# Kernel optimization log

Hardware: AMD Instinct MI355X
Metric: run time of the kernel (lower is better)

Reference implementation:

```python
import jax, jax.numpy as jnp
import numpy as np


def setup_inputs() -> dict:
    key = jax.random.key(0)
    ks = jax.random.split(key, 9)
    B, D_in, H, C = 32768, 784, 256, 10
    def lin(k, fan_in, shape):
        return jax.random.normal(k, shape, dtype=jnp.float32) / np.sqrt(fan_in).astype(np.float32)
    return {
        "x": jax.random.normal(ks[0], (B, D_in), dtype=jnp.float32),
        "W1": lin(ks[1], D_in, (H, D_in)),
        "b1": lin(ks[2], D_in, (H,)),
        "W2": lin(ks[3], H, (H, H)),
        "b2": lin(ks[4], H, (H,)),
        "W3": lin(ks[5], H, (H, H)),
        "b3": lin(ks[6], H, (H,)),
        "W4": lin(ks[7], H, (C, H)),
        "b4": lin(ks[8], H, (C,)),
    }


def reference(x, W1, b1, W2, b2, W3, b3, W4, b4):
    # MLPHeb.forward_with_coactivations:
    #   prev_act = (input > 0); at each activation point (after each ReLU and
    #   at the final Linear), curr_act = (x > 0) and coactivation buffer
    #   accumulates sum_s outer(prev_act[s], curr_act[s]) == prev_act.T @ curr_act.
    act = lambda t: (t > 0).astype(t.dtype)

    a0 = act(x)                              # [B, 784]
    h1 = jax.nn.relu(x @ W1.T + b1)          # [B, 256]
    a1 = act(h1)
    c0 = a0.T @ a1                           # [784, 256]

    h2 = jax.nn.relu(h1 @ W2.T + b2)
    a2 = act(h2)
    c1 = a1.T @ a2                           # [256, 256]

    h3 = jax.nn.relu(h2 @ W3.T + b3)
    a3 = act(h3)
    c2 = a2.T @ a3                           # [256, 256]

    logits = h3 @ W4.T + b4                  # [B, 10] (last layer counts as activation point)
    a4 = act(logits)
    c3 = a3.T @ a4                           # [256, 10]

    return logits, c0, c1, c2, c3
```

## Files before the change

kernel.cpp:

```cpp
#include <hip/hip_runtime.h>
#include <hip/hip_bf16.h>

typedef unsigned short u16;
typedef unsigned long long u64;
typedef __bf16 bf16x8 __attribute__((ext_vector_type(8)));
typedef float f32x4 __attribute__((ext_vector_type(4)));

__device__ __forceinline__ void async16(const void* g, void* l) {
  __builtin_amdgcn_global_load_lds((const __attribute__((address_space(1))) void*)g,
                                   (__attribute__((address_space(3))) void*)l, 16, 0, 0);
}
__device__ __forceinline__ u16 f2bf(float f) {
  __hip_bfloat16 h = __float2bfloat16(f);
  u16 u; __builtin_memcpy(&u, &h, 2); return u;
}

__global__ __launch_bounds__(256) void convert_all(
    const float* __restrict__ W1, const float* __restrict__ W2,
    const float* __restrict__ W3, const float* __restrict__ W4,
    u16* __restrict__ w1b, u16* __restrict__ w2b,
    u16* __restrict__ w3b, u16* __restrict__ w4b) {
  int bx = blockIdx.x;
  const float* src; u16* dst; int R, C, Cp, base;
  if (bx < 800)       { src = W1; dst = w1b; R = 256; C = 784; Cp = 800; base = 0; }
  else if (bx < 1056) { src = W2; dst = w2b; R = 256; C = 256; Cp = 256; base = 800; }
  else if (bx < 1312) { src = W3; dst = w3b; R = 256; C = 256; Cp = 256; base = 1056; }
  else                { src = W4; dst = w4b; R = 10;  C = 256; Cp = 256; base = 1312; }
  int idx = (bx - base) * 256 + threadIdx.x;
  int r = idx / Cp, c = idx - r * Cp;
  float v = (r < R && c < C) ? src[(size_t)r * C + c] : 0.0f;
  dst[idx] = f2bf(v);
}

__global__ __launch_bounds__(512, 4) void fwd_fused(
    const float* __restrict__ x,
    const u16* __restrict__ W1b, const float* __restrict__ b1,
    const u16* __restrict__ W2b, const float* __restrict__ b2,
    const u16* __restrict__ W3b, const float* __restrict__ b3,
    const u16* __restrict__ W4b, const float* __restrict__ b4,
    float* __restrict__ out,
    u64* __restrict__ bits0, u64* __restrict__ bits1,
    u64* __restrict__ bits2, u64* __restrict__ bits3,
    u64* __restrict__ bits4) {

  __shared__ __align__(16) u16 hbuf[8 * 64 * 40];
  __shared__ __align__(16) u16 Wt[2][256 * 32];
  __shared__ __align__(16) float Ls[64 * 12];

  const int tid = threadIdx.x;
  const int lane = tid & 63, wv = tid >> 6;
  const int lm = lane & 15, q = lane >> 4;
  const int m0 = blockIdx.x * 64;
  const int wm = (wv & 1) * 32;
  const int wn = (wv >> 1) * 64;

  auto stageW = [&](const u16* W, int K, int kc, u16* dst) {
    #pragma unroll
    for (int i = 0; i < 2; i++) {
      int seg = i * 512 + tid;
      int n = seg >> 2, kq = seg & 3;
      async16(W + (size_t)n * K + kc * 32 + kq * 8, dst + seg * 8);
    }
  };
  auto stageW4 = [&]() {
    if (tid < 512) async16(W4b + tid * 8, Wt[1] + tid * 8);
  };
  auto epilogue = [&](f32x4 (&acc)[2][4], const float* __restrict__ bias) {
    #pragma unroll
    for (int mi = 0; mi < 2; mi++) {
      int row = wm + mi * 16 + lm;
      #pragma unroll
      for (int ni = 0; ni < 4; ni++) {
        int col = wn + ni * 16 + q * 4;
        float4 bv = *(const float4*)(bias + col);
        float h0 = acc[mi][ni][0] + bv.x; h0 = h0 > 0.0f ? h0 : 0.0f;
        float h1 = acc[mi][ni][1] + bv.y; h1 = h1 > 0.0f ? h1 : 0.0f;
        float h2 = acc[mi][ni][2] + bv.z; h2 = h2 > 0.0f ? h2 : 0.0f;
        float h3 = acc[mi][ni][3] + bv.w; h3 = h3 > 0.0f ? h3 : 0.0f;
        ushort4 o = {f2bf(h0), f2bf(h1), f2bf(h2), f2bf(h3)};
        int kt = col >> 5, cin = col & 31;
        *(ushort4*)(hbuf + kt * 2560 + row * 40 + cin) = o;
      }
    }
  };
  auto ballot_pass = [&](u64* bits) {
    u64 my = 0;
    #pragma unroll
    for (int g = 0; g < 4; g++) {
      ushort4 v0 = *(const ushort4*)(hbuf + wv * 2560 + lane * 40 + g * 8);
      ushort4 v1 = *(const ushort4*)(hbuf + wv * 2560 + lane * 40 + g * 8 + 4);
      u16 s[8] = {v0.x, v0.y, v0.z, v0.w, v1.x, v1.y, v1.z, v1.w};
      #pragma unroll
      for (int j = 0; j < 8; j++) {
        u64 m = __ballot(s[j] != 0);
        if (lane == g * 8 + j) my = m;
      }
    }
    if (lane < 32) bits[(size_t)blockIdx.x * 256 + wv * 32 + lane] = my;
  };

  {
    f32x4 acc[2][4] = {};
    float4 xv[2][2];
    bf16x8 hA[2];
    const int arow = m0 + wm + lm;

    auto loadX = [&](int kc) {
      int col = kc * 32 + q * 8;
      bool ok = col + 7 < 784;
      #pragma unroll
      for (int mi = 0; mi < 2; mi++) {
        if (ok) {
          const float* src = x + (size_t)(arow + mi * 16) * 784 + col;
          xv[mi][0] = *(const float4*)src;
          xv[mi][1] = *(const float4*)(src + 4);
        } else {
          xv[mi][0] = float4{0, 0, 0, 0};
          xv[mi][1] = float4{0, 0, 0, 0};
        }
      }
    };
    auto cvtX = [&]() {
      #pragma unroll
      for (int mi = 0; mi < 2; mi++) {
        union { bf16x8 v; u16 s[8]; } u;
        u.s[0] = f2bf(xv[mi][0].x); u.s[1] = f2bf(xv[mi][0].y);
        u.s[2] = f2bf(xv[mi][0].z); u.s[3] = f2bf(xv[mi][0].w);
        u.s[4] = f2bf(xv[mi][1].x); u.s[5] = f2bf(xv[mi][1].y);
        u.s[6] = f2bf(xv[mi][1].z); u.s[7] = f2bf(xv[mi][1].w);
        hA[mi] = u.v;
      }
    };
    auto emitBits0 = [&](int kc) {
      if (wv >= 2) return;
      u16* b16 = (u16*)bits0;
      #pragma unroll
      for (int mi = 0; mi < 2; mi++) {
        union { bf16x8 v; short s[8]; } u; u.v = hA[mi];
        int piece = (wm + mi * 16) >> 4;
        #pragma unroll
        for (int j = 0; j < 8; j++) {
          u64 m = __ballot(u.s[j] > 0);
          int col = kc * 32 + q * 8 + j;
          if (lm == j && col < 784)
            b16[((size_t)blockIdx.x * 784 + col) * 4 + piece] = (u16)(m >> (q * 16));
        }
      }
    };

    stageW(W1b, 800, 0, Wt[0]);
    loadX(0);
    cvtX();
    for (int kc = 0; kc < 25; kc++) {
      int cur = kc & 1;
      __syncthreads();
      if (kc < 24) { stageW(W1b, 800, kc + 1, Wt[1 - cur]); loadX(kc + 1); }
      else         { stageW(W2b, 256, 0, Wt[1]); }
      bf16x8 w[4];
      #pragma unroll
      for (int ni = 0; ni < 4; ni++) w[ni] = *(const bf16x8*)(Wt[cur] + (wn + ni * 16 + lm) * 32 + q * 8);
      #pragma unroll
      for (int mi = 0; mi < 2; mi++)
        #pragma unroll
        for (int ni = 0; ni < 4; ni++)
          acc[mi][ni] = __builtin_amdgcn_mfma_f32_16x16x32_bf16(w[ni], hA[mi], acc[mi][ni], 0, 0, 0);
      emitBits0(kc);
      if (kc < 24) cvtX();
    }
    __syncthreads();
    epilogue(acc, b1);
  }
  __syncthreads();
  ballot_pass(bits1);

  auto layer256 = [&](const u16* Wthis, const u16* Wnext, bool nextIsW4,
                      const float* __restrict__ bias, u64* bits) {
    f32x4 acc[2][4] = {};
    for (int kc = 0; kc < 8; kc++) {
      int cur = (kc & 1) ^ 1;
      __syncthreads();
      if (kc < 7)       stageW(Wthis, 256, kc + 1, Wt[cur ^ 1]);
      else if (nextIsW4) stageW4();
      else              stageW(Wnext, 256, 0, Wt[cur ^ 1]);
      bf16x8 w[4], h[2];
      #pragma unroll
      for (int ni = 0; ni < 4; ni++) w[ni] = *(const bf16x8*)(Wt[cur] + (wn + ni * 16 + lm) * 32 + q * 8);
      #pragma unroll
      for (int mi = 0; mi < 2; mi++) h[mi] = *(const bf16x8*)(hbuf + kc * 2560 + (wm + mi * 16 + lm) * 40 + q * 8);
      #pragma unroll
      for (int mi = 0; mi < 2; mi++)
        #pragma unroll
        for (int ni = 0; ni < 4; ni++)
          acc[mi][ni] = __builtin_amdgcn_mfma_f32_16x16x32_bf16(w[ni], h[mi], acc[mi][ni], 0, 0, 0);
    }
    __syncthreads();
    epilogue(acc, bias);
    __syncthreads();
    ballot_pass(bits);
  };
  layer256(W2b, W3b, false, b2, bits2);
  layer256(W3b, W4b, true,  b3, bits3);

  if (wv < 4) {
    const int r0 = wv * 16;
    f32x4 acc = {};
    #pragma unroll
    for (int kc = 0; kc < 8; kc++) {
      bf16x8 wf = *(const bf16x8*)(Wt[1] + lm * 256 + kc * 32 + q * 8);
      bf16x8 hf = *(const bf16x8*)(hbuf + kc * 2560 + (r0 + lm) * 40 + q * 8);
      acc = __builtin_amdgcn_mfma_f32_16x16x32_bf16(wf, hf, acc, 0, 0, 0);
    }
    int row = r0 + lm;
    float4 v;
    #pragma unroll
    for (int r = 0; r < 4; r++) {
      int c = q * 4 + r;
      float bv = (c < 10) ? b4[c] : 0.0f;
      v[r] = acc[r] + bv;
    }
    if (q < 3) *(float4*)(Ls + row * 12 + q * 4) = v;
    size_t ob = (size_t)(m0 + row) * 10;
    if (q < 2) {
      *(float2*)(out + ob + q * 4)     = make_float2(v[0], v[1]);
      *(float2*)(out + ob + q * 4 + 2) = make_float2(v[2], v[3]);
    } else if (q == 2) {
      *(float2*)(out + ob + 8) = make_float2(v[0], v[1]);
    }
  }
  __syncthreads();
  if (wv == 0) {
    float4 c03 = *(const float4*)(Ls + lane * 12);
    float4 c47 = *(const float4*)(Ls + lane * 12 + 4);
    float2 c89 = *(const float2*)(Ls + lane * 12 + 8);
    float s[10] = {c03.x, c03.y, c03.z, c03.w, c47.x, c47.y, c47.z, c47.w, c89.x, c89.y};
    u64 my = 0;
    #pragma unroll
    for (int c = 0; c < 10; c++) {
      u64 m = __ballot(s[c] > 0.0f);
      if (lane == c) my = m;
    }
    if (lane < 10) bits4[(size_t)blockIdx.x * 10 + lane] = my;
  }
}

__global__ __launch_bounds__(256) void coact_all(
    const u64* __restrict__ bits0, const u64* __restrict__ bits1,
    const u64* __restrict__ bits2, const u64* __restrict__ bits3,
    const u64* __restrict__ bits4, float* __restrict__ out) {
  const int bx = blockIdx.x;
  const u64 *bp, *bc; float* Cm; int FP, FC, i0, j0;
  if (bx < 52)      { bp = bits0; bc = bits1; Cm = out + 327680; FP = 784; FC = 256;
                      i0 = (bx % 13) * 64; j0 = (bx / 13) * 64; }
  else if (bx < 68) { int t = bx - 52; bp = bits1; bc = bits2; Cm = out + 528384; FP = 256; FC = 256;
                      i0 = (t & 3) * 64; j0 = (t >> 2) * 64; }
  else if (bx < 84) { int t = bx - 68; bp = bits2; bc = bits3; Cm = out + 593920; FP = 256; FC = 256;
                      i0 = (t & 3) * 64; j0 = (t >> 2) * 64; }
  else              { int t = bx - 84; bp = bits3; bc = bits4; Cm = out + 659456; FP = 256; FC = 10;
                      i0 = t * 64; j0 = 0; }

  __shared__ u64 Ps[16 * 64];
  __shared__ u64 Cs[16 * 64];
  const int tid = threadIdx.x;
  const int ch0 = blockIdx.y * 32;
  const int ti = tid >> 4, tj = tid & 15;
  unsigned cnt[4][4] = {};

  for (int s = 0; s < 2; s++) {
    int cb = ch0 + s * 16;
    #pragma unroll
    for (int r = 0; r < 4; r++) {
      int l = r * 256 + tid;
      int c = l >> 6, f = l & 63;
      Ps[l] = (i0 + f < FP) ? bp[(size_t)(cb + c) * FP + i0 + f] : 0ULL;
      Cs[l] = (j0 + f < FC) ? bc[(size_t)(cb + c) * FC + j0 + f] : 0ULL;
    }
    __syncthreads();
    #pragma unroll 4
    for (int c = 0; c < 16; c++) {
      u64 pv[4], cv[4];
      #pragma unroll
      for (int a = 0; a < 4; a++) pv[a] = Ps[c * 64 + a * 16 + ti];
      #pragma unroll
      for (int b = 0; b < 4; b++) cv[b] = Cs[c * 64 + b * 16 + tj];
      #pragma unroll
      for (int a = 0; a < 4; a++)
        #pragma unroll
        for (int b = 0; b < 4; b++)
          cnt[a][b] += (unsigned)__builtin_popcountll(pv[a] & cv[b]);
    }
    __syncthreads();
  }

  #pragma unroll
  for (int a = 0; a < 4; a++) {
    int i = i0 + a * 16 + ti;
    if (i >= FP) continue;
    #pragma unroll
    for (int b = 0; b < 4; b++) {
      int j = j0 + b * 16 + tj;
      if (j < FC) atomicAdd(&Cm[(size_t)i * FC + j], (float)cnt[a][b]);
    }
  }
}

extern "C" void kernel_launch(void* const* d_in, const int* in_sizes, int n_in,
                              void* d_out, int out_size, void* d_ws, size_t ws_size,
                              hipStream_t stream) {
  const float* x  = (const float*)d_in[0];
  const float* W1 = (const float*)d_in[1];
  const float* b1 = (const float*)d_in[2];
  const float* W2 = (const float*)d_in[3];
  const float* b2 = (const float*)d_in[4];
  const float* W3 = (const float*)d_in[5];
  const float* b3 = (const float*)d_in[6];
  const float* W4 = (const float*)d_in[7];
  const float* b4 = (const float*)d_in[8];
  float* out = (float*)d_out;

  constexpr size_t O_C0 = 327680, O_END = 662016;

  char* p = (char*)d_ws;
  u16* w1b  = (u16*)p;  p += (size_t)256 * 800 * 2;
  u16* w2b  = (u16*)p;  p += (size_t)256 * 256 * 2;
  u16* w3b  = (u16*)p;  p += (size_t)256 * 256 * 2;
  u16* w4b  = (u16*)p;  p += (size_t)16 * 256 * 2;
  u64* bits0 = (u64*)p; p += (size_t)512 * 784 * 8;
  u64* bits1 = (u64*)p; p += (size_t)512 * 256 * 8;
  u64* bits2 = (u64*)p; p += (size_t)512 * 256 * 8;
  u64* bits3 = (u64*)p; p += (size_t)512 * 256 * 8;
  u64* bits4 = (u64*)p; p += (size_t)512 * 10 * 8;

  hipMemsetAsync((void*)(out + O_C0), 0, (O_END - O_C0) * sizeof(float), stream);

  convert_all<<<1328, 256, 0, stream>>>(W1, W2, W3, W4, w1b, w2b, w3b, w4b);

  fwd_fused<<<512, 512, 0, stream>>>(x, w1b, b1, w2b, b2, w3b, b3, w4b, b4,
                                     out, bits0, bits1, bits2, bits3, bits4);

  coact_all<<<dim3(88, 16), 256, 0, stream>>>(bits0, bits1, bits2, bits3, bits4, out);
}
```

Baseline: 258.4 us.

## Prefetch x two chunks ahead and spread layer-0 ballot work across all waves

The layer-1 loop now double-buffers the fp32 x register loads so each chunk is fetched two iterations before it is converted, giving global loads more time to land. The bits0 ballot emission, previously done only by waves 0-1 over all 8 columns, is split so every wave handles two columns, balancing that work across the block. This costs extra registers for the second x buffer, which may lower occupancy.

```diff
diff --git a/kernel.cpp b/kernel.cpp
--- a/kernel.cpp
+++ b/kernel.cpp
@@ -101,45 +101,46 @@
 
   {
     f32x4 acc[2][4] = {};
-    float4 xv[2][2];
+    float4 xv[2][2][2];
     bf16x8 hA[2];
     const int arow = m0 + wm + lm;
 
-    auto loadX = [&](int kc) {
+    auto loadX = [&](int kc, int buf) {
       int col = kc * 32 + q * 8;
       bool ok = col + 7 < 784;
       #pragma unroll
       for (int mi = 0; mi < 2; mi++) {
         if (ok) {
           const float* src = x + (size_t)(arow + mi * 16) * 784 + col;
-          xv[mi][0] = *(const float4*)src;
-          xv[mi][1] = *(const float4*)(src + 4);
+          xv[buf][mi][0] = *(const float4*)src;
+          xv[buf][mi][1] = *(const float4*)(src + 4);
         } else {
-          xv[mi][0] = float4{0, 0, 0, 0};
-          xv[mi][1] = float4{0, 0, 0, 0};
+          xv[buf][mi][0] = float4{0, 0, 0, 0};
+          xv[buf][mi][1] = float4{0, 0, 0, 0};
         }
       }
     };
-    auto cvtX = [&]() {
+    auto cvtX = [&](int buf) {
       #pragma unroll
       for (int mi = 0; mi < 2; mi++) {
         union { bf16x8 v; u16 s[8]; } u;
-        u.s[0] = f2bf(xv[mi][0].x); u.s[1] = f2bf(xv[mi][0].y);
-        u.s[2] = f2bf(xv[mi][0].z); u.s[3] = f2bf(xv[mi][0].w);
-        u.s[4] = f2bf(xv[mi][1].x); u.s[5] = f2bf(xv[mi][1].y);
-        u.s[6] = f2bf(xv[mi][1].z); u.s[7] = f2bf(xv[mi][1].w);
+        u.s[0] = f2bf(xv[buf][mi][0].x); u.s[1] = f2bf(xv[buf][mi][0].y);
+        u.s[2] = f2bf(xv[buf][mi][0].z); u.s[3] = f2bf(xv[buf][mi][0].w);
+        u.s[4] = f2bf(xv[buf][mi][1].x); u.s[5] = f2bf(xv[buf][mi][1].y);
+        u.s[6] = f2bf(xv[buf][mi][1].z); u.s[7] = f2bf(xv[buf][mi][1].w);
         hA[mi] = u.v;
       }
     };
     auto emitBits0 = [&](int kc) {
-      if (wv >= 2) return;
       u16* b16 = (u16*)bits0;
+      const int jbase = (wv >> 1) * 2;
       #pragma unroll
       for (int mi = 0; mi < 2; mi++) {
         union { bf16x8 v; short s[8]; } u; u.v = hA[mi];
-        int piece = (wm + mi * 16) >> 4;
+        int piece = (wv & 1) * 2 + mi;
         #pragma unroll
-        for (int j = 0; j < 8; j++) {
+        for (int jj = 0; jj < 2; jj++) {
+          int j = jbase + jj;
           u64 m = __ballot(u.s[j] > 0);
           int col = kc * 32 + q * 8 + j;
           if (lm == j && col < 784)
@@ -149,13 +150,15 @@
     };
 
     stageW(W1b, 800, 0, Wt[0]);
-    loadX(0);
-    cvtX();
+    loadX(0, 0);
+    loadX(1, 1);
+    cvtX(0);
     for (int kc = 0; kc < 25; kc++) {
       int cur = kc & 1;
       __syncthreads();
-      if (kc < 24) { stageW(W1b, 800, kc + 1, Wt[1 - cur]); loadX(kc + 1); }
-      else         { stageW(W2b, 256, 0, Wt[1]); }
+      if (kc < 24) stageW(W1b, 800, kc + 1, Wt[1 - cur]);
+      else         stageW(W2b, 256, 0, Wt[1]);
+      if (kc < 23) loadX(kc + 2, kc & 1);
       bf16x8 w[4];
       #pragma unroll
       for (int ni = 0; ni < 4; ni++) w[ni] = *(const bf16x8*)(Wt[cur] + (wn + ni * 16 + lm) * 32 + q * 8);
@@ -165,7 +168,7 @@
         for (int ni = 0; ni < 4; ni++)
           acc[mi][ni] = __builtin_amdgcn_mfma_f32_16x16x32_bf16(w[ni], hA[mi], acc[mi][ni], 0, 0, 0);
       emitBits0(kc);
-      if (kc < 24) cvtX();
+      if (kc < 24) cvtX((kc + 1) & 1);
     }
     __syncthreads();
     epilogue(acc, b1);
```

After: 435.3 us. 1.68x slower.
